# Optimization experiments

Measured on AMD Instinct MI355X. Metric: run time of the kernel, lower is better.

The kernel has to match this reference:

```python
import jax, jax.numpy as jnp
import numpy as np

B, S, D, H, L, V, P = 4, 1024, 768, 12, 6, 50257, 1024
Dh = D // H
DF = 4 * D
LN_EPS = 1e-5


def _ln(x, g, b):
    mu = jnp.mean(x, axis=-1, keepdims=True)
    var = jnp.mean(jnp.square(x - mu), axis=-1, keepdims=True)
    return (x - mu) * jax.lax.rsqrt(var + LN_EPS) * g + b


def setup_inputs() -> dict:
    key = jax.random.key(0)
    ks = jax.random.split(key, 12)
    init = lambda k, shape: (jax.random.normal(k, shape, jnp.float32) * 0.02)
    inp = {
        'input_ids': jax.random.randint(ks[0], (B, S), 0, V).astype(jnp.int32),
        'remaining_frames_ids': jax.random.randint(ks[1], (B, S), 0, V).astype(jnp.int32),
        'wte': init(ks[2], (V, D)),
        'wte_rf': init(ks[3], (V, D)),
        'wpe': init(ks[4], (P, D)),
        'ln1_g': jnp.ones((L, D), jnp.float32), 'ln1_b': jnp.zeros((L, D), jnp.float32),
        'attn_w': init(ks[5], (L, D, 3 * D)), 'attn_b': jnp.zeros((L, 3 * D), jnp.float32),
        'proj_w': init(ks[6], (L, D, D)), 'proj_b': jnp.zeros((L, D), jnp.float32),
        'ln2_g': jnp.ones((L, D), jnp.float32), 'ln2_b': jnp.zeros((L, D), jnp.float32),
        'fc_w': init(ks[7], (L, D, DF)), 'fc_b': jnp.zeros((L, DF), jnp.float32),
        'fc2_w': init(ks[8], (L, DF, D)), 'fc2_b': jnp.zeros((L, D), jnp.float32),
        'lnf_g': jnp.ones((D,), jnp.float32), 'lnf_b': jnp.zeros((D,), jnp.float32),
    }
    return inp


def _block(h, lg1, lb1, aw, ab, pw, pb, lg2, lb2, fw, fb, f2w, f2b, causal):
    a = _ln(h, lg1, lb1)
    qkv = jnp.einsum('bsd,de->bse', a, aw) + ab          # [B,S,3D]
    q, k, v = jnp.split(qkv, 3, axis=-1)
    split = lambda t: t.reshape(B, S, H, Dh).transpose(0, 2, 1, 3)  # [B,H,S,Dh]
    q, k, v = split(q), split(k), split(v)
    w = jnp.einsum('bhqd,bhkd->bhqk', q, k) / jnp.sqrt(jnp.asarray(Dh, q.dtype))
    w = w * causal - 10000.0 * (1.0 - causal)
    w = jax.nn.softmax(w, axis=-1)
    o = jnp.einsum('bhqk,bhkd->bhqd', w, v)
    o = o.transpose(0, 2, 1, 3).reshape(B, S, D)
    o = jnp.einsum('bsd,de->bse', o, pw) + pb
    h = h + o
    m = _ln(h, lg2, lb2)
    m = jax.nn.gelu(jnp.einsum('bsd,df->bsf', m, fw) + fb, approximate=True)
    m = jnp.einsum('bsf,fd->bsd', m, f2w) + f2b
    return h + m


def reference(input_ids, remaining_frames_ids, wte, wte_rf, wpe,
              ln1_g, ln1_b, attn_w, attn_b, proj_w, proj_b,
              ln2_g, ln2_b, fc_w, fc_b, fc2_w, fc2_b, lnf_g, lnf_b):
    h = wte[input_ids] + wte_rf[remaining_frames_ids] + wpe[:S][None, :, :]
    i = jnp.arange(S)[:, None]
    j = jnp.arange(S)[None, :]
    causal = (i >= j).astype(h.dtype)[None, None, :, :]   # nd == ns
    for l in range(L):
        h = _block(h, ln1_g[l], ln1_b[l], attn_w[l], attn_b[l], proj_w[l], proj_b[l],
                   ln2_g[l], ln2_b[l], fc_w[l], fc_b[l], fc2_w[l], fc2_b[l], causal)
    return _ln(h, lnf_g, lnf_b)
```

## Files before the change

### kernel.cpp

```cpp
#include <hip/hip_runtime.h>
#include <hip/hip_bf16.h>
#include <math.h>

#define BB 4
#define SS 1024
#define DD 768
#define HH 12
#define NLAYER 6
#define DHH 64
#define DFF 3072
#define D3 2304
#define LN_EPS 1e-5f

typedef __hip_bfloat16 bf16;
typedef short bf16x8 __attribute__((ext_vector_type(8)));
typedef float f32x4 __attribute__((ext_vector_type(4)));

__device__ __forceinline__ void gload_lds16(const void* g, void* l) {
  __builtin_amdgcn_global_load_lds(
      (const __attribute__((address_space(1))) void*)g,
      (__attribute__((address_space(3))) void*)l, 16, 0, 0);
}

__device__ __forceinline__ unsigned short f2bf_bits(float x) {
  bf16 h = __float2bfloat16(x);
  union { bf16 h; unsigned short u; } c; c.h = h; return c.u;
}

__global__ __launch_bounds__(256) void embed_kernel(
    const int* __restrict__ ids, const int* __restrict__ rf,
    const float* __restrict__ wte, const float* __restrict__ wte_rf,
    const float* __restrict__ wpe, float* __restrict__ h)
{
  int idx = blockIdx.x * 256 + threadIdx.x;
  int token = idx / (DD / 4);
  int c4 = (idx % (DD / 4)) * 4;
  int s = token % SS;
  int id  = ids[token];
  int rid = rf[token];
  float4 a = *(const float4*)(wte    + (size_t)id  * DD + c4);
  float4 b = *(const float4*)(wte_rf + (size_t)rid * DD + c4);
  float4 c = *(const float4*)(wpe    + (size_t)s   * DD + c4);
  float4 o;
  o.x = a.x + b.x + c.x;
  o.y = a.y + b.y + c.y;
  o.z = a.z + b.z + c.z;
  o.w = a.w + b.w + c.w;
  *(float4*)(h + (size_t)token * DD + c4) = o;
}

__global__ __launch_bounds__(256) void transpose_cast(
    const float* __restrict__ W, bf16* __restrict__ Wt, int K, int N)
{
  __shared__ float tile[32][33];
  int n0 = blockIdx.x * 32, k0 = blockIdx.y * 32;
  int tx = threadIdx.x & 31, ty = threadIdx.x >> 5;
  #pragma unroll
  for (int i = 0; i < 4; ++i)
    tile[ty + 8 * i][tx] = W[(size_t)(k0 + ty + 8 * i) * N + n0 + tx];
  __syncthreads();
  #pragma unroll
  for (int i = 0; i < 4; ++i)
    Wt[(size_t)(n0 + ty + 8 * i) * K + k0 + tx] = __float2bfloat16(tile[tx][ty + 8 * i]);
}

__global__ __launch_bounds__(256) void vtrans_kernel(
    const bf16* __restrict__ qkv, bf16* __restrict__ vt)
{
  __shared__ unsigned short tile[32][34];
  int bh = blockIdx.z, b = bh / HH, h = bh % HH;
  int s0 = blockIdx.x * 32, d0 = blockIdx.y * 32;
  int tx = threadIdx.x & 31, ty = threadIdx.x >> 5;
  const unsigned short* src =
      (const unsigned short*)qkv + (size_t)b * SS * D3 + 2 * DD + h * DHH;
  #pragma unroll
  for (int i = 0; i < 4; ++i)
    tile[ty + 8 * i][tx] = src[(size_t)(s0 + ty + 8 * i) * D3 + d0 + tx];
  __syncthreads();
  unsigned short* dst = (unsigned short*)vt + (size_t)bh * DHH * SS;
  #pragma unroll
  for (int i = 0; i < 4; ++i)
    dst[(size_t)(d0 + ty + 8 * i) * SS + s0 + tx] = tile[tx][ty + 8 * i];
}

template <typename OutT>
__global__ __launch_bounds__(192) void ln_kernel(
    const float* __restrict__ x, const float* __restrict__ g,
    const float* __restrict__ bb, OutT* __restrict__ y)
{
  __shared__ float red[2][3];
  int row = blockIdx.x;
  int t = threadIdx.x;
  const float* xr = x + (size_t)row * DD;
  float4 v = *(const float4*)(xr + t * 4);
  float s  = v.x + v.y + v.z + v.w;
  float sq = v.x * v.x + v.y * v.y + v.z * v.z + v.w * v.w;
  #pragma unroll
  for (int off = 32; off > 0; off >>= 1) {
    s  += __shfl_down(s, off);
    sq += __shfl_down(sq, off);
  }
  int wave = t >> 6, lane = t & 63;
  if (lane == 0) { red[0][wave] = s; red[1][wave] = sq; }
  __syncthreads();
  s  = red[0][0] + red[0][1] + red[0][2];
  sq = red[1][0] + red[1][1] + red[1][2];
  float mu   = s * (1.0f / DD);
  float var  = sq * (1.0f / DD) - mu * mu;
  float rstd = rsqrtf(var + LN_EPS);
  float4 gv = *(const float4*)(g  + t * 4);
  float4 bv = *(const float4*)(bb + t * 4);
  float o0 = (v.x - mu) * rstd * gv.x + bv.x;
  float o1 = (v.y - mu) * rstd * gv.y + bv.y;
  float o2 = (v.z - mu) * rstd * gv.z + bv.z;
  float o3 = (v.w - mu) * rstd * gv.w + bv.w;
  if constexpr (sizeof(OutT) == 4) {
    float4 o = {o0, o1, o2, o3};
    *(float4*)((float*)y + (size_t)row * DD + t * 4) = o;
  } else {
    ushort4 o = {f2bf_bits(o0), f2bf_bits(o1), f2bf_bits(o2), f2bf_bits(o3)};
    *(ushort4*)((unsigned short*)y + (size_t)row * DD + t * 4) = o;
  }
}

__device__ __forceinline__ float gelu_f(float x) {
  float x3 = x * x * x;
  return 0.5f * x * (1.0f + tanhf(0.7978845608028654f * (x + 0.044715f * x3)));
}

template <int MODE, typename OutT>
__global__ __launch_bounds__(256) void gemm_bf16(
    const bf16* __restrict__ A,
    const bf16* __restrict__ Wt,
    const float* __restrict__ bias,
    const float* __restrict__ R,
    OutT* __restrict__ C, int M, int N, int K)
{
  __shared__ alignas(16) unsigned short As[4][128][8];
  __shared__ alignas(16) unsigned short Bs[4][128][8];
  const int t = threadIdx.x;
  const int lane = t & 63, wid = t >> 6;
  const int wr = wid >> 1, wc = wid & 1;
  const int bm = blockIdx.y * 128, bn = blockIdx.x * 128;

  f32x4 acc[4][4] = {};

  const int c0 = t, c1 = t + 256;
  const unsigned short* Ag0 = (const unsigned short*)A + (size_t)(bm + (c0 & 127)) * K + (c0 >> 7) * 8;
  const unsigned short* Ag1 = (const unsigned short*)A + (size_t)(bm + (c1 & 127)) * K + (c1 >> 7) * 8;
  const unsigned short* Bg0 = (const unsigned short*)Wt + (size_t)(bn + (c0 & 127)) * K + (c0 >> 7) * 8;
  const unsigned short* Bg1 = (const unsigned short*)Wt + (size_t)(bn + (c1 & 127)) * K + (c1 >> 7) * 8;
  char* AsB = (char*)As;
  char* BsB = (char*)Bs;

  const int abase = (lane >> 4) * 2048 + (wr * 64 + (lane & 15)) * 16;
  const int bbase = (lane >> 4) * 2048 + (wc * 64 + (lane & 15)) * 16;

  for (int k0 = 0; k0 < K; k0 += 32) {
    gload_lds16(Ag0 + k0, AsB + c0 * 16);
    gload_lds16(Ag1 + k0, AsB + c1 * 16);
    gload_lds16(Bg0 + k0, BsB + c0 * 16);
    gload_lds16(Bg1 + k0, BsB + c1 * 16);
    __syncthreads();

    bf16x8 a[4], b[4];
    #pragma unroll
    for (int m = 0; m < 4; ++m) a[m] = *(const bf16x8*)(AsB + abase + m * 256);
    #pragma unroll
    for (int n = 0; n < 4; ++n) b[n] = *(const bf16x8*)(BsB + bbase + n * 256);
    #pragma unroll
    for (int m = 0; m < 4; ++m)
      #pragma unroll
      for (int n = 0; n < 4; ++n)
        acc[m][n] = __builtin_amdgcn_mfma_f32_16x16x32_bf16(a[m], b[n], acc[m][n], 0, 0, 0);
    __syncthreads();
  }

  const int colg = lane & 15, rowg = (lane >> 4) * 4;
  #pragma unroll
  for (int m = 0; m < 4; ++m) {
    #pragma unroll
    for (int n = 0; n < 4; ++n) {
      int col = bn + wc * 64 + n * 16 + colg;
      float bv = bias[col];
      #pragma unroll
      for (int r = 0; r < 4; ++r) {
        int row = bm + wr * 64 + m * 16 + rowg + r;
        float v = acc[m][n][r] + bv;
        if constexpr (MODE == 1) v += R[(size_t)row * N + col];
        if constexpr (MODE == 2) v = gelu_f(v);
        if constexpr (sizeof(OutT) == 4) ((float*)C)[(size_t)row * N + col] = v;
        else ((bf16*)C)[(size_t)row * N + col] = __float2bfloat16(v);
      }
    }
  }
}

__global__ __launch_bounds__(256) void attn_mfma(
    const bf16* __restrict__ qkv,
    const bf16* __restrict__ vt,
    bf16* __restrict__ o)
{
  __shared__ unsigned short plds[4][16][40];
  const int bid = blockIdx.x;
  const int swz = (bid & 7) * 96 + (bid >> 3);
  const int bh = swz >> 4, qt = swz & 15;
  const int b = bh / HH, h = bh % HH;
  const int w = threadIdx.x >> 6, lane = threadIdx.x & 63;
  const int g = lane >> 4, l15 = lane & 15;
  const int q0 = qt * 64 + w * 16;
  const int qg = q0 + l15;

  const bf16* qbase = qkv + (size_t)b * SS * D3 + h * DHH;
  const bf16* kbase = qbase + DD;
  const bf16* vbase = vt + (size_t)bh * DHH * SS;

  bf16x8 qf0 = *(const bf16x8*)(qbase + (size_t)(q0 + l15) * D3 + g * 8);
  bf16x8 qf1 = *(const bf16x8*)(qbase + (size_t)(q0 + l15) * D3 + 32 + g * 8);

  f32x4 oacc[4] = {};
  float m = -1e30f, l = 0.f;
  const int kvend = q0 + 16;

  for (int kv0 = 0; kv0 < kvend; kv0 += 32) {
    f32x4 st[2];
    #pragma unroll
    for (int tt = 0; tt < 2; ++tt) {
      const bf16* kr = kbase + (size_t)(kv0 + tt * 16 + l15) * D3 + g * 8;
      bf16x8 kf0 = *(const bf16x8*)kr;
      bf16x8 kf1 = *(const bf16x8*)(kr + 32);
      f32x4 z = {0.f, 0.f, 0.f, 0.f};
      z = __builtin_amdgcn_mfma_f32_16x16x32_bf16(kf0, qf0, z, 0, 0, 0);
      z = __builtin_amdgcn_mfma_f32_16x16x32_bf16(kf1, qf1, z, 0, 0, 0);
      st[tt] = z;
    }
    float sv[8];
    #pragma unroll
    for (int tt = 0; tt < 2; ++tt)
      #pragma unroll
      for (int r = 0; r < 4; ++r) {
        int kv = kv0 + tt * 16 + 4 * g + r;
        float x = st[tt][r] * 0.125f;
        sv[tt * 4 + r] = (kv > qg) ? -1e30f : x;
      }
    float pmax = sv[0];
    #pragma unroll
    for (int i = 1; i < 8; ++i) pmax = fmaxf(pmax, sv[i]);
    pmax = fmaxf(pmax, __shfl_xor(pmax, 16));
    pmax = fmaxf(pmax, __shfl_xor(pmax, 32));
    float mnew = fmaxf(m, pmax);
    float alpha = __expf(m - mnew);
    float rsum = 0.f;
    ushort4 pA, pB;
    {
      float p0 = __expf(sv[0] - mnew), p1 = __expf(sv[1] - mnew);
      float p2 = __expf(sv[2] - mnew), p3 = __expf(sv[3] - mnew);
      float p4 = __expf(sv[4] - mnew), p5 = __expf(sv[5] - mnew);
      float p6 = __expf(sv[6] - mnew), p7 = __expf(sv[7] - mnew);
      rsum = ((p0 + p1) + (p2 + p3)) + ((p4 + p5) + (p6 + p7));
      pA.x = f2bf_bits(p0); pA.y = f2bf_bits(p1); pA.z = f2bf_bits(p2); pA.w = f2bf_bits(p3);
      pB.x = f2bf_bits(p4); pB.y = f2bf_bits(p5); pB.z = f2bf_bits(p6); pB.w = f2bf_bits(p7);
    }
    rsum += __shfl_xor(rsum, 16);
    rsum += __shfl_xor(rsum, 32);
    l = l * alpha + rsum; m = mnew;
    #pragma unroll
    for (int blk = 0; blk < 4; ++blk)
      #pragma unroll
      for (int r = 0; r < 4; ++r) oacc[blk][r] *= alpha;

    *(ushort4*)&plds[w][l15][4 * g]      = pA;
    *(ushort4*)&plds[w][l15][16 + 4 * g] = pB;
    asm volatile("s_waitcnt lgkmcnt(0)" ::: "memory");
    __builtin_amdgcn_sched_barrier(0);

    bf16x8 pf = *(const bf16x8*)&plds[w][l15][g * 8];
    #pragma unroll
    for (int blk = 0; blk < 4; ++blk) {
      bf16x8 vf = *(const bf16x8*)(vbase + (size_t)(blk * 16 + l15) * SS + kv0 + g * 8);
      oacc[blk] = __builtin_amdgcn_mfma_f32_16x16x32_bf16(vf, pf, oacc[blk], 0, 0, 0);
    }
  }

  float linv = 1.0f / l;
  unsigned short* ob = (unsigned short*)o + (size_t)(b * SS + qg) * DD + h * DHH;
  #pragma unroll
  for (int blk = 0; blk < 4; ++blk) {
    ushort4 ov = {f2bf_bits(oacc[blk][0] * linv), f2bf_bits(oacc[blk][1] * linv),
                  f2bf_bits(oacc[blk][2] * linv), f2bf_bits(oacc[blk][3] * linv)};
    *(ushort4*)(ob + blk * 16 + 4 * g) = ov;
  }
}

extern "C" void kernel_launch(void* const* d_in, const int* in_sizes, int n_in,
                              void* d_out, int out_size, void* d_ws, size_t ws_size,
                              hipStream_t stream)
{
  (void)in_sizes; (void)n_in; (void)out_size; (void)ws_size;
  const int*   ids    = (const int*)d_in[0];
  const int*   rfids  = (const int*)d_in[1];
  const float* wte    = (const float*)d_in[2];
  const float* wte_rf = (const float*)d_in[3];
  const float* wpe    = (const float*)d_in[4];
  const float* ln1_g  = (const float*)d_in[5];
  const float* ln1_b  = (const float*)d_in[6];
  const float* attn_w = (const float*)d_in[7];
  const float* attn_b = (const float*)d_in[8];
  const float* proj_w = (const float*)d_in[9];
  const float* proj_b = (const float*)d_in[10];
  const float* ln2_g  = (const float*)d_in[11];
  const float* ln2_b  = (const float*)d_in[12];
  const float* fc_w   = (const float*)d_in[13];
  const float* fc_b   = (const float*)d_in[14];
  const float* fc2_w  = (const float*)d_in[15];
  const float* fc2_b  = (const float*)d_in[16];
  const float* lnf_g  = (const float*)d_in[17];
  const float* lnf_b  = (const float*)d_in[18];

  const int T = BB * SS;
  const size_t TD = (size_t)T * DD;
  float* h    = (float*)d_ws;
  bf16*  qkvb = (bf16*)(h + TD);
  bf16*  vtb  = qkvb + (size_t)T * D3;
  bf16*  ff   = qkvb;
  bf16*  a    = vtb + TD;
  bf16*  att  = a;
  bf16*  awt  = a + TD;
  bf16*  pwt  = awt + (size_t)D3 * DD;
  bf16*  fwt  = pwt + (size_t)DD * DD;
  bf16*  f2wt = fwt + (size_t)DFF * DD;

  embed_kernel<<<dim3((T * DD / 4) / 256), 256, 0, stream>>>(ids, rfids, wte, wte_rf, wpe, h);

  for (int l = 0; l < NLAYER; ++l) {
    transpose_cast<<<dim3(D3 / 32,  DD / 32),  256, 0, stream>>>(attn_w + (size_t)l * DD * D3,  awt,  DD,  D3);
    transpose_cast<<<dim3(DD / 32,  DD / 32),  256, 0, stream>>>(proj_w + (size_t)l * DD * DD,  pwt,  DD,  DD);
    transpose_cast<<<dim3(DFF / 32, DD / 32),  256, 0, stream>>>(fc_w   + (size_t)l * DD * DFF, fwt,  DD,  DFF);
    transpose_cast<<<dim3(DD / 32,  DFF / 32), 256, 0, stream>>>(fc2_w  + (size_t)l * DFF * DD, f2wt, DFF, DD);

    ln_kernel<bf16><<<T, 192, 0, stream>>>(h, ln1_g + (size_t)l * DD, ln1_b + (size_t)l * DD, a);
    gemm_bf16<0, bf16><<<dim3(D3 / 128, T / 128), 256, 0, stream>>>(
        a, awt, attn_b + (size_t)l * D3, nullptr, qkvb, T, D3, DD);
    vtrans_kernel<<<dim3(SS / 32, DHH / 32, BB * HH), 256, 0, stream>>>(qkvb, vtb);
    attn_mfma<<<BB * HH * (SS / 64), 256, 0, stream>>>(qkvb, vtb, att);
    gemm_bf16<1, float><<<dim3(DD / 128, T / 128), 256, 0, stream>>>(
        att, pwt, proj_b + (size_t)l * DD, h, h, T, DD, DD);
    ln_kernel<bf16><<<T, 192, 0, stream>>>(h, ln2_g + (size_t)l * DD, ln2_b + (size_t)l * DD, a);
    gemm_bf16<2, bf16><<<dim3(DFF / 128, T / 128), 256, 0, stream>>>(
        a, fwt, fc_b + (size_t)l * DFF, nullptr, ff, T, DFF, DD);
    gemm_bf16<1, float><<<dim3(DD / 128, T / 128), 256, 0, stream>>>(
        ff, f2wt, fc2_b + (size_t)l * DD, h, h, T, DD, DFF);
  }
  ln_kernel<float><<<T, 192, 0, stream>>>(h, lnf_g, lnf_b, (float*)d_out);
}
```

Measured before the change: 2.408 ms.

## Double-buffer GEMM LDS tiles, templatize tile sizes, swizzle block order

The bf16 GEMM is templated on block and wave tile sizes and now double-buffers its LDS tiles, issuing the next k-slice's global-to-LDS loads before computing the current one. It also remaps block IDs with an XCD-style swizzle, and uses 64x128 tiles for the narrow N=768 projection and fc2 GEMMs to raise the block count. The goals are to hide global load latency behind MFMA work, fill more CUs on the small-N GEMMs, and improve cache locality. It costs double the LDS per block, and the swizzle assumes the block count divides evenly by 8.

```diff
diff --git a/kernel.cpp b/kernel.cpp
--- a/kernel.cpp
+++ b/kernel.cpp
@@ -128,7 +128,7 @@
   return 0.5f * x * (1.0f + tanhf(0.7978845608028654f * (x + 0.044715f * x3)));
 }
 
-template <int MODE, typename OutT>
+template <int BM, int BN, int WM, int WN, int MODE, typename OutT>
 __global__ __launch_bounds__(256) void gemm_bf16(
     const bf16* __restrict__ A,
     const bf16* __restrict__ Wt,
@@ -136,56 +136,82 @@
     const float* __restrict__ R,
     OutT* __restrict__ C, int M, int N, int K)
 {
-  __shared__ alignas(16) unsigned short As[4][128][8];
-  __shared__ alignas(16) unsigned short Bs[4][128][8];
+  constexpr int MR = WM / 16, NR = WN / 16;
+  constexpr int WC = BN / WN;
+  constexpr int ACH = BM * 4 / 256, BCH = BN * 4 / 256;
+  constexpr int ABUF = BM * 64, BBUF = BN * 64;
+  static_assert((BM / WM) * (BN / WN) == 4, "4 waves");
+  __shared__ alignas(16) char AsB[2 * ABUF];
+  __shared__ alignas(16) char BsB[2 * BBUF];
   const int t = threadIdx.x;
   const int lane = t & 63, wid = t >> 6;
-  const int wr = wid >> 1, wc = wid & 1;
-  const int bm = blockIdx.y * 128, bn = blockIdx.x * 128;
-
-  f32x4 acc[4][4] = {};
-
-  const int c0 = t, c1 = t + 256;
-  const unsigned short* Ag0 = (const unsigned short*)A + (size_t)(bm + (c0 & 127)) * K + (c0 >> 7) * 8;
-  const unsigned short* Ag1 = (const unsigned short*)A + (size_t)(bm + (c1 & 127)) * K + (c1 >> 7) * 8;
-  const unsigned short* Bg0 = (const unsigned short*)Wt + (size_t)(bn + (c0 & 127)) * K + (c0 >> 7) * 8;
-  const unsigned short* Bg1 = (const unsigned short*)Wt + (size_t)(bn + (c1 & 127)) * K + (c1 >> 7) * 8;
-  char* AsB = (char*)As;
-  char* BsB = (char*)Bs;
-
-  const int abase = (lane >> 4) * 2048 + (wr * 64 + (lane & 15)) * 16;
-  const int bbase = (lane >> 4) * 2048 + (wc * 64 + (lane & 15)) * 16;
-
-  for (int k0 = 0; k0 < K; k0 += 32) {
-    gload_lds16(Ag0 + k0, AsB + c0 * 16);
-    gload_lds16(Ag1 + k0, AsB + c1 * 16);
-    gload_lds16(Bg0 + k0, BsB + c0 * 16);
-    gload_lds16(Bg1 + k0, BsB + c1 * 16);
-    __syncthreads();
-
-    bf16x8 a[4], b[4];
-    #pragma unroll
-    for (int m = 0; m < 4; ++m) a[m] = *(const bf16x8*)(AsB + abase + m * 256);
-    #pragma unroll
-    for (int n = 0; n < 4; ++n) b[n] = *(const bf16x8*)(BsB + bbase + n * 256);
-    #pragma unroll
-    for (int m = 0; m < 4; ++m)
+  const int wr = wid / WC, wc = wid % WC;
+  const int g = lane >> 4, l15 = lane & 15;
+
+  const int nx = gridDim.x;
+  const int nwg = nx * gridDim.y;
+  const int bid0 = blockIdx.y * nx + blockIdx.x;
+  const int bid = (bid0 & 7) * (nwg >> 3) + (bid0 >> 3);
+  const int bm = (bid / nx) * BM, bn = (bid % nx) * BN;
+
+  f32x4 acc[MR][NR] = {};
+
+  const unsigned short* Ag[ACH];
+  const unsigned short* Bg[BCH];
+  #pragma unroll
+  for (int i = 0; i < ACH; ++i) {
+    int c = t + i * 256;
+    Ag[i] = (const unsigned short*)A + (size_t)(bm + c % BM) * K + (c / BM) * 8;
+  }
+  #pragma unroll
+  for (int i = 0; i < BCH; ++i) {
+    int c = t + i * 256;
+    Bg[i] = (const unsigned short*)Wt + (size_t)(bn + c % BN) * K + (c / BN) * 8;
+  }
+
+  auto stage = [&](int buf, int k0) {
+    #pragma unroll
+    for (int i = 0; i < ACH; ++i)
+      gload_lds16(Ag[i] + k0, AsB + buf * ABUF + (t + i * 256) * 16);
+    #pragma unroll
+    for (int i = 0; i < BCH; ++i)
+      gload_lds16(Bg[i] + k0, BsB + buf * BBUF + (t + i * 256) * 16);
+  };
+
+  const int abase = g * (BM * 16) + (wr * WM + l15) * 16;
+  const int bbase = g * (BN * 16) + (wc * WN + l15) * 16;
+
+  const int nt = K / 32;
+  stage(0, 0);
+  __syncthreads();
+  for (int tk = 0; tk < nt; ++tk) {
+    const int cur = tk & 1;
+    if (tk + 1 < nt) stage(cur ^ 1, (tk + 1) * 32);
+    bf16x8 a[MR], b[NR];
+    #pragma unroll
+    for (int m = 0; m < MR; ++m)
+      a[m] = *(const bf16x8*)(AsB + cur * ABUF + abase + m * 256);
+    #pragma unroll
+    for (int n = 0; n < NR; ++n)
+      b[n] = *(const bf16x8*)(BsB + cur * BBUF + bbase + n * 256);
+    #pragma unroll
+    for (int m = 0; m < MR; ++m)
       #pragma unroll
-      for (int n = 0; n < 4; ++n)
+      for (int n = 0; n < NR; ++n)
         acc[m][n] = __builtin_amdgcn_mfma_f32_16x16x32_bf16(a[m], b[n], acc[m][n], 0, 0, 0);
     __syncthreads();
   }
 
-  const int colg = lane & 15, rowg = (lane >> 4) * 4;
-  #pragma unroll
-  for (int m = 0; m < 4; ++m) {
-    #pragma unroll
-    for (int n = 0; n < 4; ++n) {
-      int col = bn + wc * 64 + n * 16 + colg;
+  const int colg = l15, rowg = g * 4;
+  #pragma unroll
+  for (int m = 0; m < MR; ++m) {
+    #pragma unroll
+    for (int n = 0; n < NR; ++n) {
+      int col = bn + wc * WN + n * 16 + colg;
       float bv = bias[col];
       #pragma unroll
       for (int r = 0; r < 4; ++r) {
-        int row = bm + wr * 64 + m * 16 + rowg + r;
+        int row = bm + wr * WM + m * 16 + rowg + r;
         float v = acc[m][n][r] + bv;
         if constexpr (MODE == 1) v += R[(size_t)row * N + col];
         if constexpr (MODE == 2) v = gelu_f(v);
@@ -339,16 +365,16 @@
     transpose_cast<<<dim3(DD / 32,  DFF / 32), 256, 0, stream>>>(fc2_w  + (size_t)l * DFF * DD, f2wt, DFF, DD);
 
     ln_kernel<bf16><<<T, 192, 0, stream>>>(h, ln1_g + (size_t)l * DD, ln1_b + (size_t)l * DD, a);
-    gemm_bf16<0, bf16><<<dim3(D3 / 128, T / 128), 256, 0, stream>>>(
+    gemm_bf16<128, 128, 64, 64, 0, bf16><<<dim3(D3 / 128, T / 128), 256, 0, stream>>>(
         a, awt, attn_b + (size_t)l * D3, nullptr, qkvb, T, D3, DD);
     vtrans_kernel<<<dim3(SS / 32, DHH / 32, BB * HH), 256, 0, stream>>>(qkvb, vtb);
     attn_mfma<<<BB * HH * (SS / 64), 256, 0, stream>>>(qkvb, vtb, att);
-    gemm_bf16<1, float><<<dim3(DD / 128, T / 128), 256, 0, stream>>>(
+    gemm_bf16<64, 128, 32, 64, 1, float><<<dim3(DD / 128, T / 64), 256, 0, stream>>>(
         att, pwt, proj_b + (size_t)l * DD, h, h, T, DD, DD);
     ln_kernel<bf16><<<T, 192, 0, stream>>>(h, ln2_g + (size_t)l * DD, ln2_b + (size_t)l * DD, a);
-    gemm_bf16<2, bf16><<<dim3(DFF / 128, T / 128), 256, 0, stream>>>(
+    gemm_bf16<128, 128, 64, 64, 2, bf16><<<dim3(DFF / 128, T / 128), 256, 0, stream>>>(
         a, fwt, fc_b + (size_t)l * DFF, nullptr, ff, T, DFF, DD);
-    gemm_bf16<1, float><<<dim3(DD / 128, T / 128), 256, 0, stream>>>(
+    gemm_bf16<64, 128, 32, 64, 1, float><<<dim3(DD / 128, T / 64), 256, 0, stream>>>(
         ff, f2wt, fc2_b + (size_t)l * DD, h, h, T, DD, DFF);
   }
   ln_kernel<float><<<T, 192, 0, stream>>>(h, lnf_g, lnf_b, (float*)d_out);
```

After: 2.191 ms. 9.0% less time.
